# Kernel optimization log

Hardware: AMD Instinct MI355X
Metric: run time of the kernel (lower is better)

The kernel has to match this reference:

```python
import jax, jax.numpy as jnp
import numpy as np

HEAD_SIZE = 64
TOKEN_EMB = 768
BLOCK_SIZE = 4096


def setup_inputs() -> dict:
    key = jax.random.key(0)
    ks = jax.random.split(key, 7)
    s = 1.0 / np.sqrt(TOKEN_EMB)  # torch Linear default init scale
    x = jax.random.normal(ks[0], (4, BLOCK_SIZE, TOKEN_EMB), dtype=jnp.float32)
    Wk = jax.random.uniform(ks[1], (TOKEN_EMB, HEAD_SIZE), minval=-s, maxval=s, dtype=jnp.float32)
    bk = jax.random.uniform(ks[2], (HEAD_SIZE,), minval=-s, maxval=s, dtype=jnp.float32)
    Wq = jax.random.uniform(ks[3], (TOKEN_EMB, HEAD_SIZE), minval=-s, maxval=s, dtype=jnp.float32)
    bq = jax.random.uniform(ks[4], (HEAD_SIZE,), minval=-s, maxval=s, dtype=jnp.float32)
    Wv = jax.random.uniform(ks[5], (TOKEN_EMB, HEAD_SIZE), minval=-s, maxval=s, dtype=jnp.float32)
    bv = jax.random.uniform(ks[6], (HEAD_SIZE,), minval=-s, maxval=s, dtype=jnp.float32)
    return {"x": x, "Wk": Wk, "bk": bk, "Wq": Wq, "bq": bq, "Wv": Wv, "bv": bv}


def reference(x, Wk, bk, Wq, bq, Wv, bv):
    B, T, C = x.shape
    k = x @ Wk + bk  # [B, T, H]
    q = x @ Wq + bq  # [B, T, H]
    v = x @ Wv + bv  # [B, T, H]
    # NOTE: original computes k @ q^T (not q @ k^T) and scales by C**-0.5 with
    # C = token embedding size (not head size). Reproduce faithfully.
    scale = jnp.asarray(C, x.dtype) ** -0.5
    wei = jnp.einsum('bth,bsh->bts', k, q) * scale  # [B, T, T]
    causal = jnp.tril(jnp.ones((T, T), dtype=bool))
    wei = jnp.where(causal, wei, -jnp.inf)
    wei = jax.nn.softmax(wei, axis=-1)
    return jnp.einsum('bts,bsh->bth', wei, v)  # [B, T, H]
```

## Files before the change

kernel.cpp:

```cpp
#include <hip/hip_runtime.h>
#include <hip/hip_bf16.h>

#define T_SEQ 4096
#define C_EMB 768
#define HEAD  64

typedef short  short4v __attribute__((ext_vector_type(4)));
typedef short  short8  __attribute__((ext_vector_type(8)));
typedef float  floatx4 __attribute__((ext_vector_type(4)));
typedef unsigned int uint2v __attribute__((ext_vector_type(2)));

static __device__ __forceinline__ short f2bf(float v) {
    __hip_bfloat16 h = __float2bfloat16(v);
    return *reinterpret_cast<short*>(&h);
}


__global__ void wt_transpose_kernel(const float* __restrict__ Wk,
                                    const float* __restrict__ Wq,
                                    const float* __restrict__ Wv,
                                    short* __restrict__ Wf) {
    const int total = 12 * 24 * 64 * 8;
    for (int idx = blockIdx.x * blockDim.x + threadIdx.x; idx < total;
         idx += gridDim.x * blockDim.x) {
        int e    = idx & 7;
        int lane = (idx >> 3) & 63;
        int t    = idx >> 9;
        int kc   = t % 24;
        int j    = t / 24;
        int g    = j >> 2;
        int n    = (j & 3) * 16 + (lane & 15);
        int k    = kc * 32 + ((lane >> 4) & 3) * 8 + e;
        const float* W = (g == 0) ? Wk : (g == 1) ? Wq : Wv;
        Wf[idx] = f2bf(W[k * HEAD + n]);
    }
}

__global__ __launch_bounds__(256) void qkv_mfma(
    const float* __restrict__ x, const short* __restrict__ Wf,
    const float* __restrict__ bkp, const float* __restrict__ bqp,
    const float* __restrict__ bvp,
    short* __restrict__ Kf, short* __restrict__ Qf, short* __restrict__ Vf) {
    const float scale2 = 0.052058773f;
    __shared__ __align__(16) short xs[32][200];

    const int tid  = threadIdx.x;
    const int w    = tid >> 6;
    const int lane = tid & 63;
    const int ln15 = lane & 15, quad = lane >> 4;
    const int rows0 = blockIdx.x * 32;
    const int rw = (w & 1) * 16;
    const int jb = (w >> 1) * 6;

    floatx4 acc[6];
#pragma unroll
    for (int jj = 0; jj < 6; ++jj) acc[jj] = (floatx4){0.f, 0.f, 0.f, 0.f};

    for (int ch = 0; ch < 4; ++ch) {
        floatx4 stg[6];
#pragma unroll
        for (int i = 0; i < 6; ++i) {
            int o   = i * 1024 + tid * 4;
            int r   = o / 192;
            int col = o - r * 192;
            stg[i] = *(const floatx4*)(x + (size_t)(rows0 + r) * C_EMB +
                                       ch * 192 + col);
        }
#pragma unroll
        for (int i = 0; i < 6; ++i) {
            int o   = i * 1024 + tid * 4;
            int r   = o / 192;
            int col = o - r * 192;
            unsigned p01, p23;
            asm("v_cvt_pk_bf16_f32 %0, %1, %2" : "=v"(p01) : "v"(stg[i][0]), "v"(stg[i][1]));
            asm("v_cvt_pk_bf16_f32 %0, %1, %2" : "=v"(p23) : "v"(stg[i][2]), "v"(stg[i][3]));
            *(uint2v*)&xs[r][col] = (uint2v){p01, p23};
        }
        __syncthreads();

#pragma unroll
        for (int kc2 = 0; kc2 < 6; ++kc2) {
            int kcg = ch * 6 + kc2;
            short8 a = *(const short8*)&xs[rw + ln15][kc2 * 32 + quad * 8];
            short8 wf[6];
#pragma unroll
            for (int jj = 0; jj < 6; ++jj)
                wf[jj] = *(const short8*)(Wf +
                    ((size_t)((jb + jj) * 24 + kcg) * 64 + lane) * 8);
#pragma unroll
            for (int jj = 0; jj < 6; ++jj)
                acc[jj] = __builtin_amdgcn_mfma_f32_16x16x32_bf16(a, wf[jj], acc[jj], 0, 0, 0);
        }
        __syncthreads();
    }

    short* lds = &xs[0][0];
#pragma unroll
    for (int jj = 0; jj < 6; ++jj) {
        int j  = jb + jj;
        int g  = j >> 2;
        int nl = (j & 3) * 16 + ln15;
        float bias = (g == 0 ? bkp : g == 1 ? bqp : bvp)[nl];
#pragma unroll
        for (int r = 0; r < 4; ++r) {
            int rloc = rw + quad * 4 + r;
            float v = acc[jj][r] + bias;
            int off;
            short val;
            if (g == 2) {
                val = f2bf(v);
                off = 4096 + ((nl >> 4) << 9) +
                      ((((rloc >> 3) & 3) << 4) | (nl & 15)) * 8 + (rloc & 7);
            } else {
                val = (g == 0) ? f2bf(v * scale2) : f2bf(v);
                int tr = rloc & 15, kh = nl >> 5;
                int hq = (nl >> 3) & 3, he = nl & 7;
                off = (g << 11) + (((rloc >> 4) * 2 + kh) << 9) +
                      (tr | (hq << 4)) * 8 + he;
            }
            lds[off] = val;
        }
    }
    __syncthreads();

    {
        int bb = rows0 >> 12, s = rows0 & 4095;
        size_t vbase = ((size_t)bb << 18) +
                       ((size_t)((s >> 6) * 8 + ((s >> 5) & 1)) << 9);
#pragma unroll
        for (int cc = 0; cc < 3; ++cc) {
            int i = (cc * 256 + tid) * 8;
            short8 d = *(const short8*)&lds[i];
            if (i < 2048)
                *(short8*)(Kf + (size_t)rows0 * 64 + i) = d;
            else if (i < 4096)
                *(short8*)(Qf + (size_t)rows0 * 64 + (i - 2048)) = d;
            else {
                int iv = i - 4096;
                *(short8*)(Vf + vbase + (size_t)(iv >> 9) * 1024 + (iv & 511)) = d;
            }
        }
    }
}

__global__ __launch_bounds__(64) void attn_part(
    const short* __restrict__ Kf, const short* __restrict__ Qf,
    const short* __restrict__ Vf, float* __restrict__ Oacc,
    float* __restrict__ lacc) {
    __shared__ __align__(16) short Ps[32][72];

    int lane = threadIdx.x & 63;
    int ln15 = lane & 15, quad = lane >> 4;
    int g32 = blockIdx.x, c = blockIdx.y, b = blockIdx.z;
    int dtile = g32 >> 1;
    int lo = c * 8;
    if (lo > dtile) return;
    int hi = min(dtile, lo + 7);
    int base = g32 * 32;

    short8 bk[2][2];
    {
        const short* kfp = Kf + ((size_t)(b * 256 + g32 * 2) * 2) * 512 + lane * 8;
#pragma unroll
        for (int tg = 0; tg < 2; ++tg)
#pragma unroll
            for (int kh = 0; kh < 2; ++kh)
                bk[tg][kh] = *(const short8*)(kfp + (tg * 2 + kh) * 512);
    }

    floatx4 o[2][4];
#pragma unroll
    for (int tg = 0; tg < 2; ++tg)
#pragma unroll
        for (int hb = 0; hb < 4; ++hb) o[tg][hb] = (floatx4){0.f, 0.f, 0.f, 0.f};
    float ls[2] = {0.f, 0.f};

    const short* qfp = Qf + ((size_t)(b * 256 + lo * 4) * 2) * 512 + lane * 8;
    const short* vfp = Vf + ((size_t)b << 18) + (size_t)lo * 8 * 512 + lane * 8;

    short8 aqA[4][2], bvA[4][2], aqB[4][2], bvB[4][2];
#pragma unroll
    for (int sb = 0; sb < 4; ++sb)
#pragma unroll
        for (int kh = 0; kh < 2; ++kh)
            aqA[sb][kh] = *(const short8*)(qfp + (sb * 2 + kh) * 512);
#pragma unroll
    for (int hb = 0; hb < 4; ++hb)
#pragma unroll
        for (int kh = 0; kh < 2; ++kh)
            bvA[hb][kh] = *(const short8*)(vfp + (hb * 2 + kh) * 512);

    auto tile_step = [&](short8 (&aq)[4][2], short8 (&bv)[4][2],
                         short8 (&aqn)[4][2], short8 (&bvn)[4][2], int st) {
        if (st < hi) {
            int ti = st + 1 - lo;
#pragma unroll
            for (int sb = 0; sb < 4; ++sb)
#pragma unroll
                for (int kh = 0; kh < 2; ++kh)
                    aqn[sb][kh] = *(const short8*)(qfp + (size_t)ti * 4096 +
                                                   (sb * 2 + kh) * 512);
#pragma unroll
            for (int hb = 0; hb < 4; ++hb)
#pragma unroll
                for (int kh = 0; kh < 2; ++kh)
                    bvn[hb][kh] = *(const short8*)(vfp + (size_t)ti * 4096 +
                                                   (hb * 2 + kh) * 512);
        }

        floatx4 sacc[4][2];
#pragma unroll
        for (int sb = 0; sb < 4; ++sb)
#pragma unroll
            for (int tg = 0; tg < 2; ++tg) {
                floatx4 z = (floatx4){0.f, 0.f, 0.f, 0.f};
                z = __builtin_amdgcn_mfma_f32_16x16x32_bf16(aq[sb][0], bk[tg][0], z, 0, 0, 0);
                z = __builtin_amdgcn_mfma_f32_16x16x32_bf16(aq[sb][1], bk[tg][1], z, 0, 0, 0);
                sacc[sb][tg] = z;
            }

        bool diag = (st == dtile);
        int s0 = st * 64;
#pragma unroll
        for (int tg = 0; tg < 2; ++tg) {
            int tgl = base + tg * 16 + ln15;
#pragma unroll
            for (int sb = 0; sb < 4; ++sb) {
                float pv[4];
#pragma unroll
                for (int r = 0; r < 4; ++r) {
                    float p = __builtin_amdgcn_exp2f(sacc[sb][tg][r]);
                    if (diag) {
                        int sg = s0 + sb * 16 + quad * 4 + r;
                        p = (sg > tgl) ? 0.f : p;
                    }
                    pv[r] = p;
                }
                ls[tg] += (pv[0] + pv[1]) + (pv[2] + pv[3]);
                unsigned a01, a23;
                asm("v_cvt_pk_bf16_f32 %0, %1, %2" : "=v"(a01) : "v"(pv[0]), "v"(pv[1]));
                asm("v_cvt_pk_bf16_f32 %0, %1, %2" : "=v"(a23) : "v"(pv[2]), "v"(pv[3]));
                *(uint2v*)&Ps[tg * 16 + ln15][sb * 16 + quad * 4] = (uint2v){a01, a23};
            }
        }
        __asm__ volatile("s_waitcnt lgkmcnt(0)" ::: "memory");
        short8 ap[2][2];
#pragma unroll
        for (int tg = 0; tg < 2; ++tg) {
            ap[tg][0] = *(const short8*)&Ps[tg * 16 + ln15][quad * 8];
            ap[tg][1] = *(const short8*)&Ps[tg * 16 + ln15][32 + quad * 8];
        }

#pragma unroll
        for (int tg = 0; tg < 2; ++tg)
#pragma unroll
            for (int hb = 0; hb < 4; ++hb) {
                o[tg][hb] = __builtin_amdgcn_mfma_f32_16x16x32_bf16(ap[tg][0], bv[hb][0], o[tg][hb], 0, 0, 0);
                o[tg][hb] = __builtin_amdgcn_mfma_f32_16x16x32_bf16(ap[tg][1], bv[hb][1], o[tg][hb], 0, 0, 0);
            }
    };

#pragma unroll
    for (int it = 0; it < 8; it += 2) {
        if (lo + it > hi) break;
        tile_step(aqA, bvA, aqB, bvB, lo + it);
        if (lo + it + 1 > hi) break;
        tile_step(aqB, bvB, aqA, bvA, lo + it + 1);
    }

#pragma unroll
    for (int tg = 0; tg < 2; ++tg) {
        float v = ls[tg];
        v += __shfl_xor(v, 16, 64);
        v += __shfl_xor(v, 32, 64);
        if (quad == 0)
            atomicAdd(lacc + (size_t)b * T_SEQ + base + tg * 16 + ln15, v);
    }
#pragma unroll
    for (int tg = 0; tg < 2; ++tg)
#pragma unroll
        for (int r = 0; r < 4; ++r) {
            int t = base + tg * 16 + quad * 4 + r;
#pragma unroll
            for (int hb = 0; hb < 4; ++hb)
                atomicAdd(Oacc + ((size_t)(b * T_SEQ + t)) * HEAD + hb * 16 + ln15,
                          o[tg][hb][r]);
        }
}

__global__ __launch_bounds__(256) void attn_div(
    const float* __restrict__ Oacc, const float* __restrict__ lacc,
    float* __restrict__ out) {
    int idx = blockIdx.x * 256 + threadIdx.x;
    out[idx] = Oacc[idx] / lacc[idx >> 6];
}

extern "C" void kernel_launch(void* const* d_in, const int* in_sizes, int n_in,
                              void* d_out, int out_size, void* d_ws, size_t ws_size,
                              hipStream_t stream) {
    const int XSZ = 4 * T_SEQ * C_EMB;
    const int WSZ = C_EMB * HEAD;
    const int BSZ = HEAD;
    const float* x = nullptr;
    const float* W[3] = {nullptr, nullptr, nullptr};
    const float* B[3] = {nullptr, nullptr, nullptr};
    int iw = 0, ib = 0;
    for (int i = 0; i < n_in; ++i) {
        if (in_sizes[i] == XSZ) x = (const float*)d_in[i];
        else if (in_sizes[i] == WSZ && iw < 3) W[iw++] = (const float*)d_in[i];
        else if (in_sizes[i] == BSZ && ib < 3) B[ib++] = (const float*)d_in[i];
    }

    short* ws = (short*)d_ws;
    short* Kf = ws;
    short* Qf = Kf + (size_t)4 * T_SEQ * HEAD;
    short* Vf = Qf + (size_t)4 * T_SEQ * HEAD;
    short* Wf = Vf + (size_t)4 * HEAD * T_SEQ;
    float* Oacc = (float*)(Wf + (size_t)3 * HEAD * C_EMB);
    float* lacc = Oacc + (size_t)4 * T_SEQ * HEAD;

    hipMemsetAsync(Oacc, 0,
                   ((size_t)4 * T_SEQ * HEAD + 4 * T_SEQ) * sizeof(float),
                   stream);
    wt_transpose_kernel<<<96, 256, 0, stream>>>(W[0], W[1], W[2], Wf);
    qkv_mfma<<<512, 256, 0, stream>>>(x, Wf, B[0], B[1], B[2], Kf, Qf, Vf);
    attn_part<<<dim3(128, 8, 4), 64, 0, stream>>>(Kf, Qf, Vf, Oacc, lacc);
    attn_div<<<4096, 256, 0, stream>>>(Oacc, lacc, (float*)d_out);
}
```

Baseline: 155.0 us.

## Replace atomic split-K accumulation with per-chunk partial buffers reduced in divide kernel

Each attention block now writes its partial output and row-sum to a dedicated per-chunk slice instead of atomically adding into a shared accumulator. The final divide kernel sums up to eight chunk partials per row before normalizing. This drops the memset and the float atomics, at the cost of a larger workspace and more reads in the reduction kernel.

```diff
diff --git a/kernel.cpp b/kernel.cpp
--- a/kernel.cpp
+++ b/kernel.cpp
@@ -145,8 +145,8 @@
 
 __global__ __launch_bounds__(64) void attn_part(
     const short* __restrict__ Kf, const short* __restrict__ Qf,
-    const short* __restrict__ Vf, float* __restrict__ Oacc,
-    float* __restrict__ lacc) {
+    const short* __restrict__ Vf, float* __restrict__ Opart,
+    float* __restrict__ lpart) {
     __shared__ __align__(16) short Ps[32][72];
 
     int lane = threadIdx.x & 63;
@@ -268,13 +268,16 @@
         tile_step(aqB, bvB, aqA, bvA, lo + it + 1);
     }
 
+    float* op = Opart + ((size_t)(b * 8 + c) << 12) * HEAD;
+    float* lp = lpart + ((size_t)(b * 8 + c) << 12);
+
 #pragma unroll
     for (int tg = 0; tg < 2; ++tg) {
         float v = ls[tg];
         v += __shfl_xor(v, 16, 64);
         v += __shfl_xor(v, 32, 64);
         if (quad == 0)
-            atomicAdd(lacc + (size_t)b * T_SEQ + base + tg * 16 + ln15, v);
+            lp[base + tg * 16 + ln15] = v;
     }
 #pragma unroll
     for (int tg = 0; tg < 2; ++tg)
@@ -283,16 +286,25 @@
             int t = base + tg * 16 + quad * 4 + r;
 #pragma unroll
             for (int hb = 0; hb < 4; ++hb)
-                atomicAdd(Oacc + ((size_t)(b * T_SEQ + t)) * HEAD + hb * 16 + ln15,
-                          o[tg][hb][r]);
+                op[(size_t)t * HEAD + hb * 16 + ln15] = o[tg][hb][r];
         }
 }
 
 __global__ __launch_bounds__(256) void attn_div(
-    const float* __restrict__ Oacc, const float* __restrict__ lacc,
+    const float* __restrict__ Opart, const float* __restrict__ lpart,
     float* __restrict__ out) {
     int idx = blockIdx.x * 256 + threadIdx.x;
-    out[idx] = Oacc[idx] / lacc[idx >> 6];
+    int h = idx & 63;
+    int t = (idx >> 6) & 4095;
+    int b = idx >> 18;
+    int nch = (t >> 9) + 1;
+    float os = 0.f, l = 0.f;
+    for (int c = 0; c < nch; ++c) {
+        size_t s = (size_t)(b * 8 + c) << 12;
+        os += Opart[(s + t) * HEAD + h];
+        l  += lpart[s + t];
+    }
+    out[idx] = os / l;
 }
 
 extern "C" void kernel_launch(void* const* d_in, const int* in_sizes, int n_in,
@@ -316,14 +328,11 @@
     short* Qf = Kf + (size_t)4 * T_SEQ * HEAD;
     short* Vf = Qf + (size_t)4 * T_SEQ * HEAD;
     short* Wf = Vf + (size_t)4 * HEAD * T_SEQ;
-    float* Oacc = (float*)(Wf + (size_t)3 * HEAD * C_EMB);
-    float* lacc = Oacc + (size_t)4 * T_SEQ * HEAD;
-
-    hipMemsetAsync(Oacc, 0,
-                   ((size_t)4 * T_SEQ * HEAD + 4 * T_SEQ) * sizeof(float),
-                   stream);
+    float* Opart = (float*)(Wf + (size_t)3 * HEAD * C_EMB);
+    float* lpart = Opart + (size_t)32 * T_SEQ * HEAD;
+
     wt_transpose_kernel<<<96, 256, 0, stream>>>(W[0], W[1], W[2], Wf);
     qkv_mfma<<<512, 256, 0, stream>>>(x, Wf, B[0], B[1], B[2], Kf, Qf, Vf);
-    attn_part<<<dim3(128, 8, 4), 64, 0, stream>>>(Kf, Qf, Vf, Oacc, lacc);
-    attn_div<<<4096, 256, 0, stream>>>(Oacc, lacc, (float*)d_out);
-}
+    attn_part<<<dim3(128, 8, 4), 64, 0, stream>>>(Kf, Qf, Vf, Opart, lpart);
+    attn_div<<<4096, 256, 0, stream>>>(Opart, lpart, (float*)d_out);
+}
```

Result: faster. 150.1 us (-3.2%).
